# Performance work log

Hardware: AMD Instinct MI355X
Metric: run time of the kernel (lower is better)

## Reference

```python
import jax, jax.numpy as jnp
import numpy as np

N_NODES = 100000
N_EDGES = 1600000
F = 64          # node_features (in == out for EvolveGCNO)
HID = 64        # hidden_size


def setup_inputs() -> dict:
    key = jax.random.key(0)
    ks = jax.random.split(key, 12)
    s = 1.0 / np.sqrt(F)
    inp = {
        "x": jax.random.normal(ks[0], (N_NODES, F), dtype=jnp.float32),
        "edge_index": jax.random.randint(ks[1], (2, N_EDGES), 0, N_NODES, dtype=jnp.int64),
        "edge_weight": jax.random.uniform(ks[2], (N_EDGES,), dtype=jnp.float32),
        # evolving GCN weight (initial_weight of EvolveGCNO)
        "W0": jax.random.uniform(ks[3], (F, F), jnp.float32, -s, s),
        # GRU (input_size=F, hidden_size=F): gates ordered r, z, n
        "gru_Wi": jax.random.uniform(ks[4], (3 * F, F), jnp.float32, -s, s),
        "gru_Wh": jax.random.uniform(ks[5], (3 * F, F), jnp.float32, -s, s),
        "gru_bi": jax.random.uniform(ks[6], (3 * F,), jnp.float32, -s, s),
        "gru_bh": jax.random.uniform(ks[7], (3 * F,), jnp.float32, -s, s),
        # projection F -> HID and head HID -> 1
        "proj_W": jax.random.uniform(ks[8], (HID, F), jnp.float32, -s, s),
        "proj_b": jax.random.uniform(ks[9], (HID,), jnp.float32, -s, s),
        "lin_W": jax.random.uniform(ks[10], (1, HID), jnp.float32, -1.0 / np.sqrt(HID), 1.0 / np.sqrt(HID)),
        "lin_b": jax.random.uniform(ks[11], (1,), jnp.float32, -1.0 / np.sqrt(HID), 1.0 / np.sqrt(HID)),
    }
    return inp


def reference(x, edge_index, edge_weight, W0, gru_Wi, gru_Wh, gru_bi, gru_bh,
              proj_W, proj_b, lin_W, lin_b):
    N = x.shape[0]
    # --- EvolveGCNO weight evolution: one GRU step, rows of W0 are both input and hidden ---
    gi = W0 @ gru_Wi.T + gru_bi  # [F, 3F]
    gh = W0 @ gru_Wh.T + gru_bh  # [F, 3F]
    i_r, i_z, i_n = jnp.split(gi, 3, axis=1)
    h_r, h_z, h_n = jnp.split(gh, 3, axis=1)
    r = jax.nn.sigmoid(i_r + h_r)
    z = jax.nn.sigmoid(i_z + h_z)
    n = jnp.tanh(i_n + r * h_n)
    W = (1.0 - z) * n + z * W0  # evolved GCN weight [F, F]

    # --- GCNConv with fixed evolved W: X' = D^-1/2 (A + I) D^-1/2 (X W) ---
    xw = x @ W  # [N, F]
    src, dst = edge_index[0], edge_index[1]
    loop = jnp.arange(N)
    src2 = jnp.concatenate([src, loop])
    dst2 = jnp.concatenate([dst, loop])
    w2 = jnp.concatenate([edge_weight, jnp.ones((N,), xw.dtype)])  # self-loop weight 1
    deg = jax.ops.segment_sum(w2, dst2, num_segments=N)
    dinv = jnp.where(deg > 0, jax.lax.rsqrt(deg), 0.0)
    norm = dinv[src2] * w2 * dinv[dst2]  # [E + N]
    h = jax.ops.segment_sum(xw[src2] * norm[:, None], dst2, num_segments=N)  # [N, F]

    # --- MLP head (dropout is identity in eval) ---
    h = jax.nn.relu(h @ proj_W.T + proj_b)
    return h @ lin_W.T + lin_b  # [N, 1]
```

## Files before the change

### kernel.cpp

```cpp
#include <hip/hip_runtime.h>
#include <stdint.h>

#define FDIM 64
#define BINSH 6
#define NBINS 1563
#define BCAP 1536
#define OVCAP 8192
#define PSTAGE 8192
#define PBLK 196
#define GBLK 391
#define LSTRIDE 72

__device__ __forceinline__ float bf2f(unsigned int u) {
    union { float f; uint32_t i; } v; v.i = (u & 0xFFFFu) << 16; return v.f;
}
__device__ __forceinline__ unsigned short f2bf(float f) {
    union { float f; uint32_t i; } v; v.f = f;
    uint32_t u = v.i;
    u += 0x7FFFu + ((u >> 16) & 1u);
    return (unsigned short)(u >> 16);
}

__global__ __launch_bounds__(256) void k_sentinel(float* out, int N, float val) {
    int n = blockIdx.x * 256 + threadIdx.x;
    if (n < N) out[n] = (n == 0) ? val : 0.f;
}

__global__ __launch_bounds__(64) void k_gru(
    const float* __restrict__ W0, const float* __restrict__ Wi,
    const float* __restrict__ Wh, const float* __restrict__ bi,
    const float* __restrict__ bh, const float* __restrict__ projW,
    float* __restrict__ M) {
    __shared__ float w0s[64];
    __shared__ float wrow[64];
    int i = blockIdx.x, t = threadIdx.x;
    w0s[t] = W0[i * 64 + t];
    __syncthreads();
    {
        int j = t;
        float a0 = 0.f, a1 = 0.f, a2 = 0.f, b0 = 0.f, b1 = 0.f, b2 = 0.f;
#pragma unroll 8
        for (int k = 0; k < 64; k++) {
            float w0k = w0s[k];
            a0 += w0k * Wi[(j)       * 64 + k];
            a1 += w0k * Wi[(64 + j)  * 64 + k];
            a2 += w0k * Wi[(128 + j) * 64 + k];
            b0 += w0k * Wh[(j)       * 64 + k];
            b1 += w0k * Wh[(64 + j)  * 64 + k];
            b2 += w0k * Wh[(128 + j) * 64 + k];
        }
        float ir = a0 + bi[j],        hr = b0 + bh[j];
        float iz = a1 + bi[64 + j],   hz = b1 + bh[64 + j];
        float in_ = a2 + bi[128 + j], hn = b2 + bh[128 + j];
        float r = 1.f / (1.f + expf(-(ir + hr)));
        float z = 1.f / (1.f + expf(-(iz + hz)));
        float n = tanhf(in_ + r * hn);
        wrow[j] = (1.f - z) * n + z * w0s[j];
    }
    __syncthreads();
    {
        float s = 0.f;
#pragma unroll 8
        for (int q = 0; q < 64; q++) s += wrow[q] * projW[t * 64 + q];
        M[i * 64 + t] = s;
    }
}

__global__ __launch_bounds__(1024) void k_pg(
    const int* __restrict__ src, const int* __restrict__ dst,
    const float* __restrict__ ew, int* __restrict__ gcnt,
    int2* __restrict__ part, int* __restrict__ ovf_cnt,
    int* __restrict__ ovs, int* __restrict__ ovd, float* __restrict__ ovw, int E,
    const float* __restrict__ x, const float* __restrict__ M,
    unsigned short* __restrict__ xm, int N) {
    __shared__ __align__(16) char smu[123456];
    int t = threadIdx.x;
    if (blockIdx.x < PBLK) {
        int2* sorted_ = (int2*)smu;
        int*  gposa   = (int*)(smu + 65536);
        int*  hist    = (int*)(smu + 98304);
        int*  lbase   = (int*)(smu + 98304 + 6256);
        int*  lcur    = (int*)(smu + 98304 + 12512);
        int*  gboff   = (int*)(smu + 98304 + 18768);
        int*  wsum    = (int*)(smu + 98304 + 25024);
        for (int b = t; b < NBINS; b += 1024) hist[b] = 0;
        __syncthreads();
        int e0 = blockIdx.x * PSTAGE;
        int cnt = E - e0; if (cnt > PSTAGE) cnt = PSTAGE;
        for (int i = t; i < cnt; i += 1024) atomicAdd(&hist[dst[e0 + i] >> BINSH], 1);
        __syncthreads();
        for (int b = t; b < NBINS; b += 1024) {
            int h = hist[b];
            gboff[b] = h ? atomicAdd(&gcnt[b], h) : 0;
        }
        int b0i = 2 * t, b1i = 2 * t + 1;
        int h0 = (b0i < NBINS) ? hist[b0i] : 0;
        int h1 = (b1i < NBINS) ? hist[b1i] : 0;
        int c2 = h0 + h1;
        int lane = t & 63, wid = t >> 6;
        int v = c2;
#pragma unroll
        for (int d = 1; d < 64; d <<= 1) {
            int o = __shfl_up(v, d);
            if (lane >= d) v += o;
        }
        if (lane == 63) wsum[wid] = v;
        __syncthreads();
        if (t < 16) {
            int w = wsum[t];
#pragma unroll
            for (int d = 1; d < 16; d <<= 1) {
                int o = __shfl_up(w, d);
                if (t >= d) w += o;
            }
            wsum[t] = w;
        }
        __syncthreads();
        int base = (wid > 0) ? wsum[wid - 1] : 0;
        int excl = base + v - c2;
        if (b0i < NBINS) { lbase[b0i] = excl;      lcur[b0i] = excl; }
        if (b1i < NBINS) { lbase[b1i] = excl + h0; lcur[b1i] = excl + h0; }
        __syncthreads();
        for (int i = t; i < cnt; i += 1024) {
            int e = e0 + i;
            int d = dst[e];
            int b = d >> BINSH;
            int p = atomicAdd(&lcur[b], 1);
            sorted_[p] = make_int2(src[e] | ((d & 63) << 20), __float_as_int(ew[e]));
            int off = gboff[b] + (p - lbase[b]);
            if (off < BCAP) {
                gposa[p] = b * BCAP + off;
            } else {
                gposa[p] = -1;
                int op = atomicAdd(ovf_cnt, 1);
                if (op < OVCAP) { ovs[op] = src[e]; ovd[op] = d; ovw[op] = ew[e]; }
            }
        }
        __syncthreads();
        for (int j = t; j < cnt; j += 1024) {
            int g = gposa[j];
            if (g >= 0) part[g] = sorted_[j];
        }
    } else {
        int g = t >> 8, tt = t & 255;
        int tile = (blockIdx.x - PBLK) * 4 + g;
        float* ms = (float*)smu;
        float* xs = (float*)(smu + 17408 + g * 17408);
        {
            int lin = t * 4;
            *(float4*)&ms[(lin >> 6) * 68 + (lin & 63)] = *(const float4*)(M + lin);
        }
        int nb = tile * 64;
#pragma unroll
        for (int i = 0; i < 4; i++) {
            int lin = i * 1024 + tt * 4;
            int row = lin >> 6, col = lin & 63;
            int node = nb + row;
            float4 v = make_float4(0.f, 0.f, 0.f, 0.f);
            if (node < N) v = *(const float4*)(x + (size_t)node * 64 + col);
            *(float4*)&xs[row * 68 + col] = v;
        }
        __syncthreads();
        int tj = tt & 15, tn = tt >> 4;
        float acc[4][4] = {};
        for (int k = 0; k < 64; k += 4) {
            float4 xv[4], mv[4];
#pragma unroll
            for (int nn = 0; nn < 4; nn++) xv[nn] = *(const float4*)&xs[(tn * 4 + nn) * 68 + k];
#pragma unroll
            for (int kk = 0; kk < 4; kk++) mv[kk] = *(const float4*)&ms[(k + kk) * 68 + tj * 4];
#pragma unroll
            for (int nn = 0; nn < 4; nn++) {
                const float* xp = (const float*)&xv[nn];
#pragma unroll
                for (int kk = 0; kk < 4; kk++) {
                    float xk = xp[kk];
                    const float* mp = (const float*)&mv[kk];
                    acc[nn][0] += xk * mp[0];
                    acc[nn][1] += xk * mp[1];
                    acc[nn][2] += xk * mp[2];
                    acc[nn][3] += xk * mp[3];
                }
            }
        }
#pragma unroll
        for (int nn = 0; nn < 4; nn++) {
            int node = nb + tn * 4 + nn;
            if (node < N) {
                ushort4 o;
                o.x = f2bf(acc[nn][0]); o.y = f2bf(acc[nn][1]);
                o.z = f2bf(acc[nn][2]); o.w = f2bf(acc[nn][3]);
                *(ushort4*)&xm[(size_t)node * 64 + tj * 4] = o;
            }
        }
    }
}

__global__ __launch_bounds__(256) void k_deg(
    const int* __restrict__ gcnt, const int2* __restrict__ part,
    const int* __restrict__ ovf_cnt, const int* __restrict__ ovd,
    const float* __restrict__ ovw, float* __restrict__ dinv,
    int* __restrict__ loffg, int N) {
    __shared__ float dl[64];
    __shared__ int   cntl[64];
    __shared__ int   lofl[65];
    int t = threadIdx.x, b = blockIdx.x;
    if (t < 64) { dl[t] = 1.0f; cntl[t] = 0; }
    __syncthreads();
    int c = gcnt[b]; if (c > BCAP) c = BCAP;
    const int2* pe = part + (size_t)b * BCAP;
    for (int i = t; i < c; i += 256) {
        int2 e = pe[i];
        int nl = (e.x >> 20) & 63;
        atomicAdd(&dl[nl], __int_as_float(e.y));
        atomicAdd(&cntl[nl], 1);
    }
    int m = *ovf_cnt; if (m > OVCAP) m = OVCAP;
    for (int i = t; i < m; i += 256) {
        int d = ovd[i];
        if ((d >> BINSH) == b) atomicAdd(&dl[d & 63], ovw[i]);
    }
    __syncthreads();
    if (t == 0) {
        int o = 0;
#pragma unroll 16
        for (int k = 0; k < 64; k++) { lofl[k] = o; o += cntl[k]; }
        lofl[64] = o;
    }
    __syncthreads();
    if (t < 64) {
        int n = b * 64 + t;
        if (n < N) dinv[n] = rsqrtf(dl[t]);
    }
    if (t < 65) loffg[b * LSTRIDE + t] = lofl[t];
}

__global__ __launch_bounds__(256) void k_gf(
    const unsigned short* __restrict__ xm, const float* __restrict__ dinv,
    const int* __restrict__ gcnt, const int2* __restrict__ part,
    const int* __restrict__ loffg,
    const float* __restrict__ projB, const float* __restrict__ linW,
    const float* __restrict__ linB, const int* __restrict__ ovf_cnt,
    const int* __restrict__ ovs, const int* __restrict__ ovd,
    const float* __restrict__ ovw, float* __restrict__ out, int N) {
    __shared__ int  loff[65];
    __shared__ int  lcur[32];
    __shared__ int2 ledge[BCAP];
    __shared__ float pbs[64], lws[64];
    int t = threadIdx.x, hb = blockIdx.x;
    int b = hb >> 1, half = hb & 1, nl0 = half << 5;
    if (t < 65) loff[t] = loffg[b * LSTRIDE + t];
    if (t < 64) { pbs[t] = projB[t]; lws[t] = linW[t]; }
    __syncthreads();
    int base = loff[nl0];
    if (t < 32) lcur[t] = loff[nl0 + t] - base;
    __syncthreads();
    int c = gcnt[b]; if (c > BCAP) c = BCAP;
    const int2* pe = part + (size_t)b * BCAP;
    for (int i = t; i < c; i += 256) {
        int2 e = pe[i];
        int nl = (e.x >> 20) & 63;
        if ((nl >> 5) != half) continue;
        int s = e.x & 0xFFFFF;
        float nw = dinv[s] * __int_as_float(e.y);
        int p = atomicAdd(&lcur[nl & 31], 1);
        ledge[p] = make_int2(e.x, __float_as_int(nw));
    }
    __syncthreads();
    int m = *ovf_cnt; if (m > OVCAP) m = OVCAP;
    float lb = linB[0];
    int wv = t >> 6, lane = t & 63, eg = lane >> 4, fq = lane & 15, f = fq * 4;
    for (int j = wv; j < 32; j += 4) {
        int nl = nl0 + j;
        int n = b * 64 + nl;
        if (n >= N) continue;
        float dn = dinv[n];
        int beg = loff[nl] - base, end = loff[nl + 1] - base;
        float a0 = 0.f, a1 = 0.f, a2 = 0.f, a3 = 0.f;
        float b0 = 0.f, b1 = 0.f, b2 = 0.f, b3 = 0.f;
        float c0 = 0.f, c1 = 0.f, c2 = 0.f, c3 = 0.f;
        float d0 = 0.f, d1 = 0.f, d2 = 0.f, d3 = 0.f;
        int i = beg + eg;
        for (; i + 12 < end; i += 16) {
            int2 e0 = ledge[i];
            int2 e1 = ledge[i + 4];
            int2 e2 = ledge[i + 8];
            int2 e3 = ledge[i + 12];
            uint2 u0 = *(const uint2*)&xm[(size_t)(e0.x & 0xFFFFF) * 64 + f];
            uint2 u1 = *(const uint2*)&xm[(size_t)(e1.x & 0xFFFFF) * 64 + f];
            uint2 u2 = *(const uint2*)&xm[(size_t)(e2.x & 0xFFFFF) * 64 + f];
            uint2 u3 = *(const uint2*)&xm[(size_t)(e3.x & 0xFFFFF) * 64 + f];
            float w0 = __int_as_float(e0.y);
            float w1 = __int_as_float(e1.y);
            float w2 = __int_as_float(e2.y);
            float w3 = __int_as_float(e3.y);
            a0 += w0 * bf2f(u0.x); a1 += w0 * bf2f(u0.x >> 16);
            a2 += w0 * bf2f(u0.y); a3 += w0 * bf2f(u0.y >> 16);
            b0 += w1 * bf2f(u1.x); b1 += w1 * bf2f(u1.x >> 16);
            b2 += w1 * bf2f(u1.y); b3 += w1 * bf2f(u1.y >> 16);
            c0 += w2 * bf2f(u2.x); c1 += w2 * bf2f(u2.x >> 16);
            c2 += w2 * bf2f(u2.y); c3 += w2 * bf2f(u2.y >> 16);
            d0 += w3 * bf2f(u3.x); d1 += w3 * bf2f(u3.x >> 16);
            d2 += w3 * bf2f(u3.y); d3 += w3 * bf2f(u3.y >> 16);
        }
        for (; i + 4 < end; i += 8) {
            int2 e0 = ledge[i];
            int2 e1 = ledge[i + 4];
            uint2 u0 = *(const uint2*)&xm[(size_t)(e0.x & 0xFFFFF) * 64 + f];
            uint2 u1 = *(const uint2*)&xm[(size_t)(e1.x & 0xFFFFF) * 64 + f];
            float w0 = __int_as_float(e0.y);
            float w1 = __int_as_float(e1.y);
            a0 += w0 * bf2f(u0.x); a1 += w0 * bf2f(u0.x >> 16);
            a2 += w0 * bf2f(u0.y); a3 += w0 * bf2f(u0.y >> 16);
            b0 += w1 * bf2f(u1.x); b1 += w1 * bf2f(u1.x >> 16);
            b2 += w1 * bf2f(u1.y); b3 += w1 * bf2f(u1.y >> 16);
        }
        for (; i < end; i += 4) {
            int2 e0 = ledge[i];
            uint2 u0 = *(const uint2*)&xm[(size_t)(e0.x & 0xFFFFF) * 64 + f];
            float w0 = __int_as_float(e0.y);
            a0 += w0 * bf2f(u0.x); a1 += w0 * bf2f(u0.x >> 16);
            a2 += w0 * bf2f(u0.y); a3 += w0 * bf2f(u0.y >> 16);
        }
        a0 += b0 + c0 + d0; a1 += b1 + c1 + d1;
        a2 += b2 + c2 + d2; a3 += b3 + c3 + d3;
        a0 *= dn; a1 *= dn; a2 *= dn; a3 *= dn;
        a0 += __shfl_xor(a0, 16); a1 += __shfl_xor(a1, 16);
        a2 += __shfl_xor(a2, 16); a3 += __shfl_xor(a3, 16);
        a0 += __shfl_xor(a0, 32); a1 += __shfl_xor(a1, 32);
        a2 += __shfl_xor(a2, 32); a3 += __shfl_xor(a3, 32);
        if (eg == 0) {
            {
                uint2 u = *(const uint2*)&xm[(size_t)n * 64 + f];
                float sl = dn * dn;
                a0 += sl * bf2f(u.x); a1 += sl * bf2f(u.x >> 16);
                a2 += sl * bf2f(u.y); a3 += sl * bf2f(u.y >> 16);
            }
            for (int q = 0; q < m; q++) {
                if (ovd[q] == n) {
                    int s = ovs[q];
                    float nm = dinv[s] * ovw[q] * dn;
                    uint2 u = *(const uint2*)&xm[(size_t)s * 64 + f];
                    a0 += nm * bf2f(u.x); a1 += nm * bf2f(u.x >> 16);
                    a2 += nm * bf2f(u.y); a3 += nm * bf2f(u.y >> 16);
                }
            }
            float v0 = a0 + pbs[f],     v1 = a1 + pbs[f + 1];
            float v2 = a2 + pbs[f + 2], v3 = a3 + pbs[f + 3];
            float s = (v0 > 0.f ? v0 : 0.f) * lws[f]
                    + (v1 > 0.f ? v1 : 0.f) * lws[f + 1]
                    + (v2 > 0.f ? v2 : 0.f) * lws[f + 2]
                    + (v3 > 0.f ? v3 : 0.f) * lws[f + 3];
            s += __shfl_xor(s, 1); s += __shfl_xor(s, 2);
            s += __shfl_xor(s, 4); s += __shfl_xor(s, 8);
            if (fq == 0) out[n] = s + lb;
        }
    }
}

extern "C" void kernel_launch(void* const* d_in, const int* in_sizes, int n_in,
                              void* d_out, int out_size, void* d_ws, size_t ws_size,
                              hipStream_t stream) {
    const float* x   = (const float*)d_in[0];
    const int*   ei  = (const int*)d_in[1];
    const float* ew  = (const float*)d_in[2];
    const float* W0  = (const float*)d_in[3];
    const float* gWi = (const float*)d_in[4];
    const float* gWh = (const float*)d_in[5];
    const float* gbi = (const float*)d_in[6];
    const float* gbh = (const float*)d_in[7];
    const float* pW  = (const float*)d_in[8];
    const float* pb  = (const float*)d_in[9];
    const float* lW  = (const float*)d_in[10];
    const float* lb  = (const float*)d_in[11];
    float* out = (float*)d_out;

    static const int EXPSZ[12] = {6400000, 3200000, 1600000, 4096, 12288, 12288,
                                  192, 192, 4096, 64, 64, 1};
    int mism = -1;
    for (int i = 0; i < 12 && i < n_in; i++)
        if (in_sizes[i] != EXPSZ[i]) { mism = i; break; }
    if (mism >= 0) {
        k_sentinel<<<(out_size + 255) / 256, 256, 0, stream>>>(out, out_size,
                                                               ldexpf(1.f, 30 + 3 * mism));
        return;
    }

    int N = in_sizes[0] / FDIM;
    int E = in_sizes[1] / 2;
    const int* src = ei;
    const int* dst = ei + E;

    char* wsb = (char*)d_ws;
    float* M       = (float*)(wsb);
    int*   gcnt    = (int*)  (wsb + (32u << 10));
    int*   ovf_cnt = (int*)  (wsb + (39u << 10));
    int*   ovs     = (int*)  (wsb + (44u << 10));
    int*   ovd     = (int*)  (wsb + (76u << 10));
    float* ovw     = (float*)(wsb + (108u << 10));
    float* dinv    = (float*)(wsb + (1u << 20));
    int*   loffg   = (int*)  (wsb + 1572864u);
    int2*  part    = (int2*) (wsb + (2u << 20));
    unsigned short* xm = (unsigned short*)(wsb + (22u << 20));

    hipMemsetAsync(gcnt, 0, (8u << 10), stream);

    k_gru<<<64, 64, 0, stream>>>(W0, gWi, gWh, gbi, gbh, pW, M);
    k_pg<<<PBLK + GBLK, 1024, 0, stream>>>(src, dst, ew, gcnt, part,
                                           ovf_cnt, ovs, ovd, ovw, E,
                                           x, M, xm, N);
    k_deg<<<NBINS, 256, 0, stream>>>(gcnt, part, ovf_cnt, ovd, ovw,
                                     dinv, loffg, N);
    k_gf<<<NBINS * 2, 256, 0, stream>>>(xm, dinv, gcnt, part, loffg, pb, lW, lb,
                                        ovf_cnt, ovs, ovd, ovw, out, N);
}
```

Before: 196.6 us.

## Halve partition stage size, prefetch edges into registers, merge gather half-blocks

The partition/GEMM kernel now processes 4096 edges per block with twice as many blocks, cutting shared memory from about 123KB to 74KB so more blocks can be resident. Edge src/dst/weight are loaded once into registers and reused for both histogram and scatter passes instead of being reloaded from global memory. The GEMM half uses 2 tiles per block with 2 rows per thread. The gather kernel switches from two 256-thread half-bin blocks to one 512-thread block per bin, so each bin's edge list is scanned once rather than twice, in exchange for larger blocks and less parallelism granularity.

After: 659.2 us. 235% more time.

```diff
diff --git a/kernel.cpp b/kernel.cpp
--- a/kernel.cpp
+++ b/kernel.cpp
@@ -6,9 +6,9 @@
 #define NBINS 1563
 #define BCAP 1536
 #define OVCAP 8192
-#define PSTAGE 8192
-#define PBLK 196
-#define GBLK 391
+#define PSTAGE 4096
+#define PBLK 392
+#define GBLK 782
 #define LSTRIDE 72
 
 __device__ __forceinline__ float bf2f(unsigned int u) {
@@ -73,21 +73,35 @@
     int* __restrict__ ovs, int* __restrict__ ovd, float* __restrict__ ovw, int E,
     const float* __restrict__ x, const float* __restrict__ M,
     unsigned short* __restrict__ xm, int N) {
-    __shared__ __align__(16) char smu[123456];
+    __shared__ __align__(16) char smu[74240];
     int t = threadIdx.x;
     if (blockIdx.x < PBLK) {
         int2* sorted_ = (int2*)smu;
-        int*  gposa   = (int*)(smu + 65536);
-        int*  hist    = (int*)(smu + 98304);
-        int*  lbase   = (int*)(smu + 98304 + 6256);
-        int*  lcur    = (int*)(smu + 98304 + 12512);
-        int*  gboff   = (int*)(smu + 98304 + 18768);
-        int*  wsum    = (int*)(smu + 98304 + 25024);
+        int*  gposa   = (int*)(smu + 32768);
+        int*  hist    = (int*)(smu + 49152);
+        int*  lbase   = (int*)(smu + 55408);
+        int*  lcur    = (int*)(smu + 61664);
+        int*  gboff   = (int*)(smu + 67920);
+        int*  wsum    = (int*)(smu + 74176);
         for (int b = t; b < NBINS; b += 1024) hist[b] = 0;
         __syncthreads();
         int e0 = blockIdx.x * PSTAGE;
         int cnt = E - e0; if (cnt > PSTAGE) cnt = PSTAGE;
-        for (int i = t; i < cnt; i += 1024) atomicAdd(&hist[dst[e0 + i] >> BINSH], 1);
+        int   d_r[4], s_r[4];
+        float w_r[4];
+#pragma unroll
+        for (int k = 0; k < 4; k++) {
+            int i = t + (k << 10);
+            if (i < cnt) {
+                int e = e0 + i;
+                d_r[k] = dst[e]; s_r[k] = src[e]; w_r[k] = ew[e];
+            }
+        }
+#pragma unroll
+        for (int k = 0; k < 4; k++) {
+            int i = t + (k << 10);
+            if (i < cnt) atomicAdd(&hist[d_r[k] >> BINSH], 1);
+        }
         __syncthreads();
         for (int b = t; b < NBINS; b += 1024) {
             int h = hist[b];
@@ -121,19 +135,22 @@
         if (b0i < NBINS) { lbase[b0i] = excl;      lcur[b0i] = excl; }
         if (b1i < NBINS) { lbase[b1i] = excl + h0; lcur[b1i] = excl + h0; }
         __syncthreads();
-        for (int i = t; i < cnt; i += 1024) {
-            int e = e0 + i;
-            int d = dst[e];
-            int b = d >> BINSH;
-            int p = atomicAdd(&lcur[b], 1);
-            sorted_[p] = make_int2(src[e] | ((d & 63) << 20), __float_as_int(ew[e]));
-            int off = gboff[b] + (p - lbase[b]);
-            if (off < BCAP) {
-                gposa[p] = b * BCAP + off;
-            } else {
-                gposa[p] = -1;
-                int op = atomicAdd(ovf_cnt, 1);
-                if (op < OVCAP) { ovs[op] = src[e]; ovd[op] = d; ovw[op] = ew[e]; }
+#pragma unroll
+        for (int k = 0; k < 4; k++) {
+            int i = t + (k << 10);
+            if (i < cnt) {
+                int d = d_r[k];
+                int b = d >> BINSH;
+                int p = atomicAdd(&lcur[b], 1);
+                sorted_[p] = make_int2(s_r[k] | ((d & 63) << 20), __float_as_int(w_r[k]));
+                int off = gboff[b] + (p - lbase[b]);
+                if (off < BCAP) {
+                    gposa[p] = b * BCAP + off;
+                } else {
+                    gposa[p] = -1;
+                    int op = atomicAdd(ovf_cnt, 1);
+                    if (op < OVCAP) { ovs[op] = s_r[k]; ovd[op] = d; ovw[op] = w_r[k]; }
+                }
             }
         }
         __syncthreads();
@@ -142,8 +159,8 @@
             if (g >= 0) part[g] = sorted_[j];
         }
     } else {
-        int g = t >> 8, tt = t & 255;
-        int tile = (blockIdx.x - PBLK) * 4 + g;
+        int g = t >> 9, tt = t & 511;
+        int tile = (blockIdx.x - PBLK) * 2 + g;
         float* ms = (float*)smu;
         float* xs = (float*)(smu + 17408 + g * 17408);
         {
@@ -152,8 +169,8 @@
         }
         int nb = tile * 64;
 #pragma unroll
-        for (int i = 0; i < 4; i++) {
-            int lin = i * 1024 + tt * 4;
+        for (int i = 0; i < 2; i++) {
+            int lin = i * 2048 + tt * 4;
             int row = lin >> 6, col = lin & 63;
             int node = nb + row;
             float4 v = make_float4(0.f, 0.f, 0.f, 0.f);
@@ -162,15 +179,15 @@
         }
         __syncthreads();
         int tj = tt & 15, tn = tt >> 4;
-        float acc[4][4] = {};
+        float acc[2][4] = {};
         for (int k = 0; k < 64; k += 4) {
-            float4 xv[4], mv[4];
-#pragma unroll
-            for (int nn = 0; nn < 4; nn++) xv[nn] = *(const float4*)&xs[(tn * 4 + nn) * 68 + k];
+            float4 xv[2], mv[4];
+#pragma unroll
+            for (int nn = 0; nn < 2; nn++) xv[nn] = *(const float4*)&xs[(tn * 2 + nn) * 68 + k];
 #pragma unroll
             for (int kk = 0; kk < 4; kk++) mv[kk] = *(const float4*)&ms[(k + kk) * 68 + tj * 4];
 #pragma unroll
-            for (int nn = 0; nn < 4; nn++) {
+            for (int nn = 0; nn < 2; nn++) {
                 const float* xp = (const float*)&xv[nn];
 #pragma unroll
                 for (int kk = 0; kk < 4; kk++) {
@@ -184,8 +201,8 @@
             }
         }
 #pragma unroll
-        for (int nn = 0; nn < 4; nn++) {
-            int node = nb + tn * 4 + nn;
+        for (int nn = 0; nn < 2; nn++) {
+            int node = nb + tn * 2 + nn;
             if (node < N) {
                 ushort4 o;
                 o.x = f2bf(acc[nn][0]); o.y = f2bf(acc[nn][1]);
@@ -235,7 +252,7 @@
     if (t < 65) loffg[b * LSTRIDE + t] = lofl[t];
 }
 
-__global__ __launch_bounds__(256) void k_gf(
+__global__ __launch_bounds__(512) void k_gf(
     const unsigned short* __restrict__ xm, const float* __restrict__ dinv,
     const int* __restrict__ gcnt, const int2* __restrict__ part,
     const int* __restrict__ loffg,
@@ -244,38 +261,33 @@
     const int* __restrict__ ovs, const int* __restrict__ ovd,
     const float* __restrict__ ovw, float* __restrict__ out, int N) {
     __shared__ int  loff[65];
-    __shared__ int  lcur[32];
+    __shared__ int  lcur[64];
     __shared__ int2 ledge[BCAP];
     __shared__ float pbs[64], lws[64];
-    int t = threadIdx.x, hb = blockIdx.x;
-    int b = hb >> 1, half = hb & 1, nl0 = half << 5;
+    int t = threadIdx.x, b = blockIdx.x;
     if (t < 65) loff[t] = loffg[b * LSTRIDE + t];
     if (t < 64) { pbs[t] = projB[t]; lws[t] = linW[t]; }
     __syncthreads();
-    int base = loff[nl0];
-    if (t < 32) lcur[t] = loff[nl0 + t] - base;
+    if (t < 64) lcur[t] = loff[t];
     __syncthreads();
     int c = gcnt[b]; if (c > BCAP) c = BCAP;
     const int2* pe = part + (size_t)b * BCAP;
-    for (int i = t; i < c; i += 256) {
+    for (int i = t; i < c; i += 512) {
         int2 e = pe[i];
-        int nl = (e.x >> 20) & 63;
-        if ((nl >> 5) != half) continue;
         int s = e.x & 0xFFFFF;
         float nw = dinv[s] * __int_as_float(e.y);
-        int p = atomicAdd(&lcur[nl & 31], 1);
+        int p = atomicAdd(&lcur[(e.x >> 20) & 63], 1);
         ledge[p] = make_int2(e.x, __float_as_int(nw));
     }
     __syncthreads();
     int m = *ovf_cnt; if (m > OVCAP) m = OVCAP;
     float lb = linB[0];
     int wv = t >> 6, lane = t & 63, eg = lane >> 4, fq = lane & 15, f = fq * 4;
-    for (int j = wv; j < 32; j += 4) {
-        int nl = nl0 + j;
+    for (int nl = wv; nl < 64; nl += 8) {
         int n = b * 64 + nl;
         if (n >= N) continue;
         float dn = dinv[n];
-        int beg = loff[nl] - base, end = loff[nl + 1] - base;
+        int beg = loff[nl], end = loff[nl + 1];
         float a0 = 0.f, a1 = 0.f, a2 = 0.f, a3 = 0.f;
         float b0 = 0.f, b1 = 0.f, b2 = 0.f, b3 = 0.f;
         float c0 = 0.f, c1 = 0.f, c2 = 0.f, c3 = 0.f;
@@ -411,6 +423,6 @@
                                            x, M, xm, N);
     k_deg<<<NBINS, 256, 0, stream>>>(gcnt, part, ovf_cnt, ovd, ovw,
                                      dinv, loffg, N);
-    k_gf<<<NBINS * 2, 256, 0, stream>>>(xm, dinv, gcnt, part, loffg, pb, lW, lb,
-                                        ovf_cnt, ovs, ovd, ovw, out, N);
-}
+    k_gf<<<NBINS, 512, 0, stream>>>(xm, dinv, gcnt, part, loffg, pb, lW, lb,
+                                    ovf_cnt, ovs, ovd, ovw, out, N);
+}
```
